# Optimization experiments

Measured on AMD Instinct MI355X. Metric: run time of the kernel, lower is better.

The kernel has to match this reference:

```python
import jax, jax.numpy as jnp
import numpy as np

EMBED_DIM = 1024
NUM_HEADS = 16
HEAD_DIM = EMBED_DIM // NUM_HEADS
SCALE = HEAD_DIM ** -0.5


def setup_inputs() -> dict:
    key = jax.random.key(0)
    k1, k2, k3, k4, k5, k6 = jax.random.split(key, 6)
    B, Tq, Tk = 2, 2048, 2048
    std = EMBED_DIM ** -0.5
    return {
        "x_q": jax.random.normal(k1, (B, Tq, EMBED_DIM), jnp.float32),
        "x_kv": jax.random.normal(k2, (B, Tk, EMBED_DIM), jnp.float32),
        "w_q": jax.random.normal(k3, (EMBED_DIM, EMBED_DIM), jnp.float32) * std,
        "w_kv": jax.random.normal(k4, (EMBED_DIM, 2 * EMBED_DIM), jnp.float32) * std,
        "w_proj": jax.random.normal(k5, (EMBED_DIM, EMBED_DIM), jnp.float32) * std,
        "w_rel": jax.random.normal(k6, (1, NUM_HEADS), jnp.float32) * 0.02,
    }


def reference(x_q, x_kv, w_q, w_kv, w_proj, w_rel):
    B, Tq, _ = x_q.shape
    Tk = x_kv.shape[1]
    # projections
    q = x_q @ w_q                       # [B,Tq,E]
    kv = x_kv @ w_kv                    # [B,Tk,2E]
    k, v = jnp.split(kv, 2, axis=-1)

    def heads(y, T):
        return y.reshape(B, T, NUM_HEADS, HEAD_DIM).transpose(0, 2, 1, 3)

    q = heads(q, Tq)                    # [B,H,Tq,D]
    k = heads(k, Tk)
    v = heads(v, Tk)

    logits = jnp.einsum('bhqd,bhkd->bhqk', q, k) * SCALE  # [B,H,Tq,Tk]

    # relative position bias: Dense(1 -> H) applied to (pos_q - pos_k)
    rel = jnp.arange(Tq, dtype=jnp.float32)[:, None] - jnp.arange(Tk, dtype=jnp.float32)[None, :]
    bias = rel[..., None] * w_rel[0]                      # [Tq,Tk,H]
    bias = bias.transpose(2, 0, 1)[None]                  # [1,H,Tq,Tk]
    logits = logits + bias

    attn = jax.nn.softmax(logits, axis=-1)                # dropout=0 / inference -> identity
    out = jnp.einsum('bhqk,bhkd->bhqd', attn, v)          # [B,H,Tq,D]
    out = out.transpose(0, 2, 1, 3).reshape(B, Tq, EMBED_DIM)
    return out @ w_proj
```

## Files before the change

kernel.cpp:

```cpp
#include <hip/hip_runtime.h>
#include <hip/hip_bf16.h>

typedef __attribute__((ext_vector_type(8))) short short8;
typedef __attribute__((ext_vector_type(8))) __bf16 bf16x8;
typedef __attribute__((ext_vector_type(4))) float f32x4;
typedef __attribute__((ext_vector_type(8))) unsigned short ushort8v;
typedef __attribute__((ext_vector_type(4))) unsigned short ushort4v;

#define NB 2
#define TQ 2048
#define TKK 2048
#define EMB 1024
#define NH 16
#define HD 64

__device__ __forceinline__ unsigned short f2bf(float f){
  union { float f; unsigned u; } v; v.f = f;
  unsigned r = v.u + 0x7FFFu + ((v.u >> 16) & 1u);
  return (unsigned short)(r >> 16);
}

#define GLOAD_LDS16(g, l) __builtin_amdgcn_global_load_lds( \
    (const __attribute__((address_space(1))) void*)(g), \
    (__attribute__((address_space(3))) void*)(l), 16, 0, 0)

#define SWZ(row, inner) ((inner) ^ (((row)&7)<<4))

__device__ __forceinline__ void mfma16(const short8& a, const short8& b, f32x4& c){
  c = __builtin_amdgcn_mfma_f32_16x16x32_bf16(
        __builtin_bit_cast(bf16x8, a), __builtin_bit_cast(bf16x8, b), c, 0, 0, 0);
}

__device__ __forceinline__ void cvt_body(const float* __restrict__ in,
    unsigned short* __restrict__ out, int i){
  float4 v = ((const float4*)in)[i];
  ushort4v o;
  o.x = f2bf(v.x); o.y = f2bf(v.y); o.z = f2bf(v.z); o.w = f2bf(v.w);
  ((ushort4v*)out)[i] = o;
}

__device__ __forceinline__ void wt_body(const float* __restrict__ W,
    unsigned short* __restrict__ WT, int K, int N, int k0, int n0,
    unsigned short (*tile)[72]){
  int tid = threadIdx.x;
  #pragma unroll
  for (int it=0; it<4; ++it){
    int c = tid + it*256;
    int r = c>>4, c4 = (c&15)*4;
    float4 v = *(const float4*)(W + (long)(k0+r)*N + n0 + c4);
    tile[r][c4+0]=f2bf(v.x); tile[r][c4+1]=f2bf(v.y);
    tile[r][c4+2]=f2bf(v.z); tile[r][c4+3]=f2bf(v.w);
  }
  __syncthreads();
  #pragma unroll
  for (int it=0; it<2; ++it){
    int c = tid + it*256;
    int n = c>>3, k8 = (c&7)*8;
    ushort8v o;
    #pragma unroll
    for (int j=0;j<8;++j) o[j] = tile[k8+j][n];
    *(ushort8v*)(WT + (long)(n0+n)*K + k0 + k8) = o;
  }
}

__global__ __launch_bounds__(256) void prep_kernel(
    const float* __restrict__ x_q, const float* __restrict__ x_kv,
    const float* __restrict__ w_q, const float* __restrict__ w_kv,
    const float* __restrict__ w_proj,
    unsigned short* __restrict__ Aq,  unsigned short* __restrict__ Akv,
    unsigned short* __restrict__ WqT, unsigned short* __restrict__ WkvT,
    unsigned short* __restrict__ WpT){
  __shared__ unsigned short tile[64][72];
  const int bx = blockIdx.x;
  if (bx < 4096){
    cvt_body(x_q, Aq, bx*256 + threadIdx.x);
  } else if (bx < 8192){
    cvt_body(x_kv, Akv, (bx-4096)*256 + threadIdx.x);
  } else if (bx < 8448){
    int blk = bx - 8192;
    wt_body(w_q, WqT, EMB, EMB, (blk>>4)*64, (blk&15)*64, tile);
  } else if (bx < 8960){
    int blk = bx - 8448;
    wt_body(w_kv, WkvT, EMB, 2*EMB, (blk>>5)*64, (blk&31)*64, tile);
  } else {
    int blk = bx - 8960;
    wt_body(w_proj, WpT, EMB, EMB, (blk>>4)*64, (blk&15)*64, tile);
  }
}

__global__ __launch_bounds__(256) void v_transpose(const unsigned short* __restrict__ KV,
    unsigned short* __restrict__ VT){
  __shared__ unsigned short tile[64][72];
  int bh = blockIdx.y; int b = bh>>4, h = bh&15;
  int t0 = blockIdx.x*64;
  int tid = threadIdx.x;
  #pragma unroll
  for (int it=0; it<2; ++it){
    int c = tid + it*256;
    int r = c>>3, d8 = (c&7)*8;
    ushort8v v = *(const ushort8v*)(KV + (long)(b*TKK + t0 + r)*(2*EMB) + EMB + h*HD + d8);
    #pragma unroll
    for (int j=0;j<8;++j) tile[r][d8+j] = v[j];
  }
  __syncthreads();
  #pragma unroll
  for (int it=0; it<2; ++it){
    int c = tid + it*256;
    int d = c>>3, t8 = (c&7)*8;
    ushort8v o;
    #pragma unroll
    for (int j=0;j<8;++j) o[j] = tile[t8+j][d];
    *(ushort8v*)(VT + (long)(bh*HD + d)*TKK + t0 + t8) = o;
  }
}

template<int OUT_BF16>
__device__ __forceinline__ void gemm_body(const unsigned short* __restrict__ A,
    const unsigned short* __restrict__ BT, void* __restrict__ Cout,
    int M, int N, int K, int m0, int n0,
    unsigned short* Al, unsigned short* Bl){
  const int tid = threadIdx.x;
  const int wave = tid>>6, lane = tid&63;
  const int wm = (wave>>1)*64, wn = (wave&1)*64;
  const int g = lane>>4, lr = lane&15;
  const int srow = lane>>3;
  const int sinner = (lane&7)*16;
  f32x4 acc[4][4] = {};

  for (int k0=0; k0<K; k0+=64){
    #pragma unroll
    for (int j=0;j<4;++j){
      int chunk = wave*4 + j;
      int row = chunk*8 + srow;
      int kb = SWZ(row, sinner);
      GLOAD_LDS16(A + (long)(m0+row)*K + k0 + (kb>>1), Al + chunk*512);
      GLOAD_LDS16(BT + (long)(n0+row)*K + k0 + (kb>>1), Bl + chunk*512);
    }
    __syncthreads();
    #pragma unroll
    for (int kk=0;kk<2;++kk){
      short8 af[4], bfr[4];
      const int kbyte = kk*64 + g*16;
      #pragma unroll
      for (int i=0;i<4;++i){
        int ar = wm + i*16 + lr;
        af[i] = *(const short8*)((const char*)Al + ar*128 + SWZ(ar, kbyte));
        int br = wn + i*16 + lr;
        bfr[i] = *(const short8*)((const char*)Bl + br*128 + SWZ(br, kbyte));
      }
      #pragma unroll
      for (int i=0;i<4;++i)
        #pragma unroll
        for (int jn=0;jn<4;++jn)
          mfma16(af[i], bfr[jn], acc[i][jn]);
    }
    __syncthreads();
  }
  #pragma unroll
  for (int i=0;i<4;++i){
    int row = m0 + wm + i*16 + g*4;
    #pragma unroll
    for (int jn=0;jn<4;++jn){
      int col = n0 + wn + jn*16 + lr;
      #pragma unroll
      for (int r=0;r<4;++r){
        if (OUT_BF16)
          ((unsigned short*)Cout)[(long)(row+r)*N + col] = f2bf(acc[i][jn][r]);
        else
          ((float*)Cout)[(long)(row+r)*N + col] = acc[i][jn][r];
      }
    }
  }
}

template<int OUT_BF16>
__global__ __launch_bounds__(256,3) void gemm_bt(const unsigned short* __restrict__ A,
    const unsigned short* __restrict__ BT, void* __restrict__ Cout,
    int M, int N, int K){
  __shared__ unsigned short Al[128*64];
  __shared__ unsigned short Bl[128*64];
  gemm_body<OUT_BF16>(A, BT, Cout, M, N, K, blockIdx.y*128, blockIdx.x*128, Al, Bl);
}

__global__ __launch_bounds__(256,3) void gemm_qkv(
    const unsigned short* __restrict__ Aq,  const unsigned short* __restrict__ WqT,  unsigned short* __restrict__ Qb,
    const unsigned short* __restrict__ Akv, const unsigned short* __restrict__ WkvT, unsigned short* __restrict__ KVb){
  __shared__ unsigned short Al[128*64];
  __shared__ unsigned short Bl[128*64];
  const int x = blockIdx.x;
  if (x < 8)
    gemm_body<1>(Aq,  WqT,  Qb,  NB*TQ, EMB,   EMB, blockIdx.y*128, x*128,     Al, Bl);
  else
    gemm_body<1>(Akv, WkvT, KVb, NB*TKK, 2*EMB, EMB, blockIdx.y*128, (x-8)*128, Al, Bl);
}

__global__ __launch_bounds__(512,4) void attn_kernel(const unsigned short* __restrict__ Qb,
    const unsigned short* __restrict__ KVb, const unsigned short* __restrict__ VT,
    const float* __restrict__ w_rel, unsigned short* __restrict__ Ob){
  __shared__ unsigned short Kl[2][64*64];
  __shared__ unsigned short Vl[2][64*64];
  __shared__ __attribute__((aligned(16))) char Pl[8][16*128];
  const int id  = blockIdx.x + 16*blockIdx.y;
  const int nid = (id & 7)*64 + (id >> 3);
  const int qb  = nid & 15, bh = nid >> 4;
  const int b = bh>>4, h = bh&15;
  const int q0 = qb*128;
  const int tid = threadIdx.x, wave = tid>>6, lane = tid&63;
  const int g = lane>>4, lr = lane&15;
  const int srow = lane>>3, sinner = (lane&7)*16;
  const float C1 = 0.125f*1.44269504f;
  const float wr2 = w_rel[h]*1.44269504f;
  const float w64 = 64.0f*wr2;
  char* Pw = &Pl[wave][0];

  const int strow = wave*8 + srow;
  const int skb = SWZ(strow, sinner);
  const unsigned short* Kg = KVb + (long)(b*TKK + strow)*(2*EMB) + h*HD + (skb>>1);
  const unsigned short* Vg = VT + (long)(bh*HD + strow)*TKK + (skb>>1);

  short8 qf[2];
  #pragma unroll
  for (int kk=0;kk<2;++kk)
    qf[kk] = *(const short8*)(Qb + (long)(b*TQ + q0 + wave*16 + lr)*EMB + h*HD + kk*32 + g*8);

  const float bq = (float)(q0 + wave*16 + lr)*wr2;
  float dq[4][4];
  #pragma unroll
  for (int n=0;n<4;++n)
    #pragma unroll
    for (int r=0;r<4;++r)
      dq[n][r] = bq - (float)(n*16 + 4*g + r)*wr2;

  short8 ones;
  #pragma unroll
  for (int j=0;j<8;++j) ones[j] = (short)0x3F80;

  f32x4 oacc[4] = {};
  f32x4 lacc = {};
  float Mxs = -1e30f;

  GLOAD_LDS16(Kg, &Kl[0][wave*512]);
  GLOAD_LDS16(Vg, &Vl[0][wave*512]);
  __syncthreads();

  int cur = 0;
  for (int kt=0; kt<TKK; kt+=64){
    if (kt + 64 < TKK){
      GLOAD_LDS16(Kg + (long)(kt+64)*(2*EMB), &Kl[cur^1][wave*512]);
      GLOAD_LDS16(Vg + (kt+64), &Vl[cur^1][wave*512]);
    }

    f32x4 sacc[4] = {};
    #pragma unroll
    for (int kk=0;kk<2;++kk){
      short8 kf[4];
      const int kbyte = kk*64 + g*16;
      #pragma unroll
      for (int n=0;n<4;++n){
        int trow = n*16 + lr;
        kf[n] = *(const short8*)((const char*)&Kl[cur][0] + trow*128 + SWZ(trow, kbyte));
      }
      #pragma unroll
      for (int n=0;n<4;++n)
        mfma16(kf[n], qf[kk], sacc[n]);
    }

    #pragma unroll
    for (int n=0;n<4;++n)
      #pragma unroll
      for (int r=0;r<4;++r)
        sacc[n][r] = fmaf(sacc[n][r], C1, dq[n][r]);

    float rowmax;
    {
      float m0 = fmaxf(fmaxf(sacc[0][0],sacc[0][1]),sacc[0][2]);
      float m1 = fmaxf(fmaxf(sacc[0][3],sacc[1][0]),sacc[1][1]);
      float m2 = fmaxf(fmaxf(sacc[1][2],sacc[1][3]),sacc[2][0]);
      float m3 = fmaxf(fmaxf(sacc[2][1],sacc[2][2]),sacc[2][3]);
      float m4 = fmaxf(fmaxf(sacc[3][0],sacc[3][1]),sacc[3][2]);
      float a  = fmaxf(fmaxf(m0,m1),m2);
      float bb = fmaxf(fmaxf(m3,m4),sacc[3][3]);
      rowmax = fmaxf(a,bb);
      rowmax = fmaxf(rowmax, __shfl_xor(rowmax, 16, 64));
      rowmax = fmaxf(rowmax, __shfl_xor(rowmax, 32, 64));
    }

    if (__any(rowmax > Mxs + 8.0f)){
      float Mn = fmaxf(Mxs, rowmax);
      float rf = exp2f(Mxs - Mn);
      Mxs = Mn;
      float rfo[4];
      #pragma unroll
      for (int r=0;r<4;++r) rfo[r] = __shfl(rf, 4*g + r, 64);
      #pragma unroll
      for (int n=0;n<4;++n)
        #pragma unroll
        for (int r=0;r<4;++r) oacc[n][r] *= rfo[r];
      #pragma unroll
      for (int r=0;r<4;++r) lacc[r] *= rfo[r];
    }

    #pragma unroll
    for (int n=0;n<4;++n){
      ushort4v w;
      #pragma unroll
      for (int r=0;r<4;++r)
        w[r] = __builtin_bit_cast(unsigned short, __float2bfloat16(exp2f(sacc[n][r]-Mxs)));
      *(ushort4v*)(Pw + lr*128 + SWZ(lr, 32*n + 8*g)) = w;
    }

    asm volatile("" ::: "memory");

    #pragma unroll
    for (int kk=0;kk<2;++kk){
      const int kbyte = kk*64 + g*16;
      short8 pf = *(const short8*)(Pw + lr*128 + SWZ(lr, kbyte));
      #pragma unroll
      for (int n=0;n<4;++n){
        int vrow = n*16 + lr;
        short8 vf = *(const short8*)((const char*)&Vl[cur][0] + vrow*128 + SWZ(vrow, kbyte));
        mfma16(pf, vf, oacc[n]);
      }
      mfma16(pf, ones, lacc);
    }

    Mxs += w64;

    __syncthreads();
    cur ^= 1;
  }

  #pragma unroll
  for (int r=0;r<4;++r){
    float inv = 1.0f / lacc[r];
    int q = q0 + wave*16 + 4*g + r;
    #pragma unroll
    for (int n=0;n<4;++n){
      int d = n*16 + lr;
      Ob[(long)(b*TQ + q)*EMB + h*HD + d] = f2bf(oacc[n][r]*inv);
    }
  }
}

extern "C" void kernel_launch(void* const* d_in, const int* in_sizes, int n_in,
                              void* d_out, int out_size, void* d_ws, size_t ws_size,
                              hipStream_t stream){
  const float* x_q    = (const float*)d_in[0];
  const float* x_kv   = (const float*)d_in[1];
  const float* w_q    = (const float*)d_in[2];
  const float* w_kv   = (const float*)d_in[3];
  const float* w_proj = (const float*)d_in[4];
  const float* w_rel  = (const float*)d_in[5];
  (void)in_sizes; (void)n_in; (void)out_size; (void)ws_size;
  char* ws = (char*)d_ws;
  const size_t MB = 1024*1024;
  unsigned short* Qb   = (unsigned short*)(ws + 0);
  unsigned short* KVb  = (unsigned short*)(ws + 8*MB);
  unsigned short* WpT  = (unsigned short*)(ws + 24*MB);
  unsigned short* WqT  = (unsigned short*)(ws + 26*MB);
  unsigned short* WkvT = (unsigned short*)(ws + 28*MB);
  unsigned short* Aq   = (unsigned short*)(ws + 32*MB);
  unsigned short* Akv  = (unsigned short*)(ws + 40*MB);
  unsigned short* Ob   = Aq;
  unsigned short* VTt  = Akv;
  float* out = (float*)d_out;

  prep_kernel<<<9216, 256, 0, stream>>>(x_q, x_kv, w_q, w_kv, w_proj,
                                        Aq, Akv, WqT, WkvT, WpT);
  gemm_qkv<<<dim3(24,32), 256, 0, stream>>>(Aq, WqT, Qb, Akv, WkvT, KVb);
  v_transpose<<<dim3(32,32), 256, 0, stream>>>(KVb, VTt);
  attn_kernel<<<dim3(16,32), 512, 0, stream>>>(Qb, KVb, VTt, w_rel, Ob);
  gemm_bt<0><<<dim3(8,32),  256, 0, stream>>>(Ob, WpT, out, NB*TQ, EMB, EMB);
}
```

Baseline: 155.4 us.

## Fuse V transpose into QKV GEMM epilogue and retile output projection

The QKV projection GEMM now writes K into its own contiguous buffer and writes V directly in the transposed per-head [b,h,d,t] layout from its epilogue. This removes the separate v_transpose kernel launch and its extra read and write of V. The attention kernel reads K with the narrower row stride. The output projection moves to a new kernel with 64x128 tiles, doubling the block count to fill more compute units, at the cost of less reuse of the weight tile per block.

```diff
diff --git a/kernel.cpp b/kernel.cpp
--- a/kernel.cpp
+++ b/kernel.cpp
@@ -88,33 +88,7 @@
   }
 }
 
-__global__ __launch_bounds__(256) void v_transpose(const unsigned short* __restrict__ KV,
-    unsigned short* __restrict__ VT){
-  __shared__ unsigned short tile[64][72];
-  int bh = blockIdx.y; int b = bh>>4, h = bh&15;
-  int t0 = blockIdx.x*64;
-  int tid = threadIdx.x;
-  #pragma unroll
-  for (int it=0; it<2; ++it){
-    int c = tid + it*256;
-    int r = c>>3, d8 = (c&7)*8;
-    ushort8v v = *(const ushort8v*)(KV + (long)(b*TKK + t0 + r)*(2*EMB) + EMB + h*HD + d8);
-    #pragma unroll
-    for (int j=0;j<8;++j) tile[r][d8+j] = v[j];
-  }
-  __syncthreads();
-  #pragma unroll
-  for (int it=0; it<2; ++it){
-    int c = tid + it*256;
-    int d = c>>3, t8 = (c&7)*8;
-    ushort8v o;
-    #pragma unroll
-    for (int j=0;j<8;++j) o[j] = tile[t8+j][d];
-    *(ushort8v*)(VT + (long)(bh*HD + d)*TKK + t0 + t8) = o;
-  }
-}
-
-template<int OUT_BF16>
+template<int MODE>
 __device__ __forceinline__ void gemm_body(const unsigned short* __restrict__ A,
     const unsigned short* __restrict__ BT, void* __restrict__ Cout,
     int M, int N, int K, int m0, int n0,
@@ -161,41 +135,110 @@
     int row = m0 + wm + i*16 + g*4;
     #pragma unroll
     for (int jn=0;jn<4;++jn){
-      int col = n0 + wn + jn*16 + lr;
-      #pragma unroll
-      for (int r=0;r<4;++r){
-        if (OUT_BF16)
-          ((unsigned short*)Cout)[(long)(row+r)*N + col] = f2bf(acc[i][jn][r]);
-        else
-          ((float*)Cout)[(long)(row+r)*N + col] = acc[i][jn][r];
-      }
-    }
-  }
-}
-
-template<int OUT_BF16>
-__global__ __launch_bounds__(256,3) void gemm_bt(const unsigned short* __restrict__ A,
-    const unsigned short* __restrict__ BT, void* __restrict__ Cout,
-    int M, int N, int K){
-  __shared__ unsigned short Al[128*64];
-  __shared__ unsigned short Bl[128*64];
-  gemm_body<OUT_BF16>(A, BT, Cout, M, N, K, blockIdx.y*128, blockIdx.x*128, Al, Bl);
+      if (MODE == 2){
+        int dg = n0 - EMB + wn + jn*16 + lr;
+        int h = dg >> 6, d = dg & 63;
+        int b = row >> 11, t = row & (TKK-1);
+        ushort4v w;
+        #pragma unroll
+        for (int r=0;r<4;++r) w[r] = f2bf(acc[i][jn][r]);
+        *(ushort4v*)((unsigned short*)Cout + ((long)((b*NH + h)*HD + d)*TKK + t)) = w;
+      } else {
+        int col = n0 + wn + jn*16 + lr;
+        #pragma unroll
+        for (int r=0;r<4;++r){
+          if (MODE == 1)
+            ((unsigned short*)Cout)[(long)(row+r)*N + col] = f2bf(acc[i][jn][r]);
+          else
+            ((float*)Cout)[(long)(row+r)*N + col] = acc[i][jn][r];
+        }
+      }
+    }
+  }
 }
 
 __global__ __launch_bounds__(256,3) void gemm_qkv(
     const unsigned short* __restrict__ Aq,  const unsigned short* __restrict__ WqT,  unsigned short* __restrict__ Qb,
-    const unsigned short* __restrict__ Akv, const unsigned short* __restrict__ WkvT, unsigned short* __restrict__ KVb){
+    const unsigned short* __restrict__ Akv, const unsigned short* __restrict__ WkvT,
+    unsigned short* __restrict__ Kb, unsigned short* __restrict__ VT){
   __shared__ unsigned short Al[128*64];
   __shared__ unsigned short Bl[128*64];
   const int x = blockIdx.x;
   if (x < 8)
-    gemm_body<1>(Aq,  WqT,  Qb,  NB*TQ, EMB,   EMB, blockIdx.y*128, x*128,     Al, Bl);
+    gemm_body<1>(Aq,  WqT,  Qb, NB*TQ, EMB, EMB, blockIdx.y*128, x*128, Al, Bl);
+  else if (x < 16)
+    gemm_body<1>(Akv, WkvT, Kb, NB*TKK, EMB, EMB, blockIdx.y*128, (x-8)*128, Al, Bl);
   else
-    gemm_body<1>(Akv, WkvT, KVb, NB*TKK, 2*EMB, EMB, blockIdx.y*128, (x-8)*128, Al, Bl);
+    gemm_body<2>(Akv, WkvT, VT, NB*TKK, EMB, EMB, blockIdx.y*128, EMB + (x-16)*128, Al, Bl);
+}
+
+__global__ __launch_bounds__(256,2) void gemm_out(const unsigned short* __restrict__ A,
+    const unsigned short* __restrict__ BT, float* __restrict__ C,
+    int M, int N, int K){
+  __shared__ unsigned short Al[64*64];
+  __shared__ unsigned short Bl[128*64];
+  const int tid = threadIdx.x;
+  const int wave = tid>>6, lane = tid&63;
+  const int m0 = blockIdx.y*64, n0 = blockIdx.x*128;
+  const int wm = (wave>>1)*32, wn = (wave&1)*64;
+  const int g = lane>>4, lr = lane&15;
+  const int srow = lane>>3;
+  const int sinner = (lane&7)*16;
+  f32x4 acc[2][4] = {};
+
+  for (int k0=0; k0<K; k0+=64){
+    #pragma unroll
+    for (int j=0;j<2;++j){
+      int chunk = wave*2 + j;
+      int row = chunk*8 + srow;
+      int kb = SWZ(row, sinner);
+      GLOAD_LDS16(A + (long)(m0+row)*K + k0 + (kb>>1), Al + chunk*512);
+    }
+    #pragma unroll
+    for (int j=0;j<4;++j){
+      int chunk = wave*4 + j;
+      int row = chunk*8 + srow;
+      int kb = SWZ(row, sinner);
+      GLOAD_LDS16(BT + (long)(n0+row)*K + k0 + (kb>>1), Bl + chunk*512);
+    }
+    __syncthreads();
+    #pragma unroll
+    for (int kk=0;kk<2;++kk){
+      short8 af[2], bfr[4];
+      const int kbyte = kk*64 + g*16;
+      #pragma unroll
+      for (int i=0;i<2;++i){
+        int ar = wm + i*16 + lr;
+        af[i] = *(const short8*)((const char*)Al + ar*128 + SWZ(ar, kbyte));
+      }
+      #pragma unroll
+      for (int jn=0;jn<4;++jn){
+        int br = wn + jn*16 + lr;
+        bfr[jn] = *(const short8*)((const char*)Bl + br*128 + SWZ(br, kbyte));
+      }
+      #pragma unroll
+      for (int i=0;i<2;++i)
+        #pragma unroll
+        for (int jn=0;jn<4;++jn)
+          mfma16(af[i], bfr[jn], acc[i][jn]);
+    }
+    __syncthreads();
+  }
+  #pragma unroll
+  for (int i=0;i<2;++i){
+    int row = m0 + wm + i*16 + g*4;
+    #pragma unroll
+    for (int jn=0;jn<4;++jn){
+      int col = n0 + wn + jn*16 + lr;
+      #pragma unroll
+      for (int r=0;r<4;++r)
+        C[(long)(row+r)*N + col] = acc[i][jn][r];
+    }
+  }
 }
 
 __global__ __launch_bounds__(512,4) void attn_kernel(const unsigned short* __restrict__ Qb,
-    const unsigned short* __restrict__ KVb, const unsigned short* __restrict__ VT,
+    const unsigned short* __restrict__ Kb, const unsigned short* __restrict__ VT,
     const float* __restrict__ w_rel, unsigned short* __restrict__ Ob){
   __shared__ unsigned short Kl[2][64*64];
   __shared__ unsigned short Vl[2][64*64];
@@ -215,7 +258,7 @@
 
   const int strow = wave*8 + srow;
   const int skb = SWZ(strow, sinner);
-  const unsigned short* Kg = KVb + (long)(b*TKK + strow)*(2*EMB) + h*HD + (skb>>1);
+  const unsigned short* Kg = Kb + (long)(b*TKK + strow)*EMB + h*HD + (skb>>1);
   const unsigned short* Vg = VT + (long)(bh*HD + strow)*TKK + (skb>>1);
 
   short8 qf[2];
@@ -246,7 +289,7 @@
   int cur = 0;
   for (int kt=0; kt<TKK; kt+=64){
     if (kt + 64 < TKK){
-      GLOAD_LDS16(Kg + (long)(kt+64)*(2*EMB), &Kl[cur^1][wave*512]);
+      GLOAD_LDS16(Kg + (long)(kt+64)*EMB, &Kl[cur^1][wave*512]);
       GLOAD_LDS16(Vg + (kt+64), &Vl[cur^1][wave*512]);
     }
 
@@ -355,20 +398,19 @@
   char* ws = (char*)d_ws;
   const size_t MB = 1024*1024;
   unsigned short* Qb   = (unsigned short*)(ws + 0);
-  unsigned short* KVb  = (unsigned short*)(ws + 8*MB);
+  unsigned short* Kb   = (unsigned short*)(ws + 8*MB);
+  unsigned short* VT   = (unsigned short*)(ws + 16*MB);
   unsigned short* WpT  = (unsigned short*)(ws + 24*MB);
   unsigned short* WqT  = (unsigned short*)(ws + 26*MB);
   unsigned short* WkvT = (unsigned short*)(ws + 28*MB);
   unsigned short* Aq   = (unsigned short*)(ws + 32*MB);
   unsigned short* Akv  = (unsigned short*)(ws + 40*MB);
   unsigned short* Ob   = Aq;
-  unsigned short* VTt  = Akv;
   float* out = (float*)d_out;
 
   prep_kernel<<<9216, 256, 0, stream>>>(x_q, x_kv, w_q, w_kv, w_proj,
                                         Aq, Akv, WqT, WkvT, WpT);
-  gemm_qkv<<<dim3(24,32), 256, 0, stream>>>(Aq, WqT, Qb, Akv, WkvT, KVb);
-  v_transpose<<<dim3(32,32), 256, 0, stream>>>(KVb, VTt);
-  attn_kernel<<<dim3(16,32), 512, 0, stream>>>(Qb, KVb, VTt, w_rel, Ob);
-  gemm_bt<0><<<dim3(8,32),  256, 0, stream>>>(Ob, WpT, out, NB*TQ, EMB, EMB);
-}
+  gemm_qkv<<<dim3(24,32), 256, 0, stream>>>(Aq, WqT, Qb, Akv, WkvT, Kb, VT);
+  attn_kernel<<<dim3(16,32), 512, 0, stream>>>(Qb, Kb, VT, w_rel, Ob);
+  gemm_out<<<dim3(8,64), 256, 0, stream>>>(Ob, WpT, out, NB*TQ, EMB, EMB);
+}
```

Result: faster. 146.1 us (-6.0%).
